# Performance work log

Measured on AMD Instinct MI355X. Metric: run time of the kernel, lower is better.

The kernel has to match this reference:

```python
import jax, jax.numpy as jnp
import numpy as np

BETA_2 = 1.0
LAMBDA_2 = 1.0


def _segment_logsumexp(x, seg, num_segments):
    # numerically stable segment logsumexp; empty segments -> 0.0
    m = jax.ops.segment_max(x, seg, num_segments=num_segments)
    m_safe = jnp.where(jnp.isfinite(m), m, 0.0)
    s = jax.ops.segment_sum(jnp.exp(x - m_safe[seg]), seg, num_segments=num_segments)
    lse = m_safe + jnp.log(s)
    return jnp.where(s > 0, lse, 0.0)


def setup_inputs() -> dict:
    key = jax.random.key(0)
    k1, k2, k3, k4, k5 = jax.random.split(key, 5)
    num_nodes, d, num_edges, num_graphs = 100000, 64, 3200000, 256
    Q2 = jax.random.normal(k1, (num_nodes, d), dtype=jnp.float32)
    K2 = jax.random.normal(k2, (num_nodes, d), dtype=jnp.float32)
    c_2 = jax.random.randint(k3, (num_edges,), 0, num_nodes)
    u_2 = jax.random.randint(k4, (num_edges,), 0, num_nodes)
    batch = jnp.sort(jax.random.randint(k5, (num_nodes,), 0, num_graphs))
    return {"Q2": Q2, "K2": K2, "c_2": c_2, "u_2": u_2, "batch": batch,
            "num_graphs": num_graphs}


def reference(Q2, K2, c_2, u_2, batch, num_graphs):
    num_nodes, d = Q2.shape
    scale = d ** 0.5
    # pairwise dot over edges: [E]
    ell_2 = jnp.sum(Q2[c_2] * K2[u_2], axis=-1) / scale
    # segment logsumexp grouped by destination node c: [N]
    lse_2 = _segment_logsumexp(BETA_2 * ell_2, c_2, num_nodes)
    # scatter-add per-node lse into per-graph energy: [G]
    graph_lse = jax.ops.segment_sum(lse_2, batch, num_segments=num_graphs)
    E = (LAMBDA_2 / BETA_2) * graph_lse
    return E
```

## Files before the change

kernel.cpp:

```cpp
#include <hip/hip_runtime.h>
#include <hip/hip_fp8.h>
#include <math.h>

typedef __attribute__((ext_vector_type(2))) float fv2;

#if defined(__has_builtin)
#  if __has_builtin(__builtin_amdgcn_cvt_pk_f32_fp8) && \
      __has_builtin(__builtin_amdgcn_cvt_pk_fp8_f32)
#    define PE_HAVE_FP8_BUILTINS 1
#  endif
#endif

#define MAX_NB 512
#define MAX_NB2 2048
#define UQ 4
#define NPB 256
#define NPB_SHIFT 8
#define B2_EPT 16
#define B2_CHUNK (B2_EPT * 256)
#define CPB 4
#define RT 1024
#define NXCD 8

__device__ __forceinline__ unsigned pack4_fp8(float a, float b, float c, float d) {
#ifdef PE_HAVE_FP8_BUILTINS
    int w = 0;
    w = __builtin_amdgcn_cvt_pk_fp8_f32(a, b, w, false);
    w = __builtin_amdgcn_cvt_pk_fp8_f32(c, d, w, true);
    return (unsigned)w;
#else
    unsigned r = 0;
    r |= (unsigned)__hip_fp8_e4m3(a).__x;
    r |= (unsigned)__hip_fp8_e4m3(b).__x << 8;
    r |= (unsigned)__hip_fp8_e4m3(c).__x << 16;
    r |= (unsigned)__hip_fp8_e4m3(d).__x << 24;
    return r;
#endif
}

__device__ __forceinline__ float dot4w_fp8(unsigned qa, unsigned ka, float acc) {
#ifdef PE_HAVE_FP8_BUILTINS
    fv2 q0 = __builtin_amdgcn_cvt_pk_f32_fp8((int)qa, false);
    fv2 q1 = __builtin_amdgcn_cvt_pk_f32_fp8((int)qa, true);
    fv2 k0 = __builtin_amdgcn_cvt_pk_f32_fp8((int)ka, false);
    fv2 k1 = __builtin_amdgcn_cvt_pk_f32_fp8((int)ka, true);
    acc = fmaf(q0.x, k0.x, acc);
    acc = fmaf(q0.y, k0.y, acc);
    acc = fmaf(q1.x, k1.x, acc);
    acc = fmaf(q1.y, k1.y, acc);
    return acc;
#else
#pragma unroll
    for (int j = 0; j < 4; ++j) {
        __hip_fp8_e4m3 qv, kv;
        qv.__x = (qa >> (8 * j)) & 0xff;
        kv.__x = (ka >> (8 * j)) & 0xff;
        acc = fmaf((float)qv, (float)kv, acc);
    }
    return acc;
#endif
}

__device__ __forceinline__ float dot16_fp8(const uint4& q, const uint4& k) {
    float d = 0.0f;
    d = dot4w_fp8(q.x, k.x, d);
    d = dot4w_fp8(q.y, k.y, d);
    d = dot4w_fp8(q.z, k.z, d);
    d = dot4w_fp8(q.w, k.w, d);
    return d;
}

__device__ __forceinline__ float red4(float d) {
    d += __shfl_xor(d, 1, 64);
    d += __shfl_xor(d, 2, 64);
    return d;
}

__device__ __forceinline__ int uquarter(int uu, int t1, int t2, int t3) {
    return (uu >= t1) + (uu >= t2) + (uu >= t3);
}

__global__ __launch_bounds__(256) void pe_convcount_kernel(
    const float* __restrict__ Q,
    const float* __restrict__ K,
    unsigned* __restrict__ Qq,
    unsigned* __restrict__ Kq,
    float* __restrict__ node_sum,
    float* __restrict__ out,
    const int* __restrict__ c,
    const int* __restrict__ u,
    unsigned* __restrict__ cnt_mat,
    int n4, int num_nodes, int num_graphs, int num_edges,
    int nb2, int nblk, int nconv,
    int t1, int t2, int t3) {
    __shared__ unsigned h[MAX_NB2];
    const int tid = threadIdx.x;

    if (blockIdx.x < nconv) {
        const int i = blockIdx.x * 256 + tid;
        if (i < num_nodes) node_sum[i] = 0.0f;
        if (i < num_graphs) out[i] = 0.0f;
        if (i >= n4) return;
        const float4 q = ((const float4*)Q)[i];
        const float4 k = ((const float4*)K)[i];
        Qq[i] = pack4_fp8(q.x, q.y, q.z, q.w);
        Kq[i] = pack4_fp8(k.x, k.y, k.z, k.w);
        return;
    }

    const int blk = blockIdx.x - nconv;
    for (int b = tid; b < nb2; b += 256) h[b] = 0u;
    __syncthreads();

    const int estart = blk * B2_CHUNK;
    const int ecount = min(B2_CHUNK, num_edges - estart);
    const int n4e = ecount >> 2;
    const int4* c4 = (const int4*)(c + estart);
    const int4* u4 = (const int4*)(u + estart);
    for (int k = tid; k < n4e; k += 256) {
        const int4 cv = c4[k];
        const int4 uv = u4[k];
        atomicAdd(&h[(cv.x >> NPB_SHIFT) * UQ + uquarter(uv.x, t1, t2, t3)], 1u);
        atomicAdd(&h[(cv.y >> NPB_SHIFT) * UQ + uquarter(uv.y, t1, t2, t3)], 1u);
        atomicAdd(&h[(cv.z >> NPB_SHIFT) * UQ + uquarter(uv.z, t1, t2, t3)], 1u);
        atomicAdd(&h[(cv.w >> NPB_SHIFT) * UQ + uquarter(uv.w, t1, t2, t3)], 1u);
    }
    for (int e = (n4e << 2) + tid; e < ecount; e += 256) {
        const int cc = c[estart + e];
        const int uu = u[estart + e];
        atomicAdd(&h[(cc >> NPB_SHIFT) * UQ + uquarter(uu, t1, t2, t3)], 1u);
    }
    __syncthreads();

    for (int b = tid; b < nb2; b += 256)
        cnt_mat[(size_t)b * nblk + blk] = h[b];
}

__global__ __launch_bounds__(256) void pe_matscan_kernel(
    unsigned* __restrict__ cnt_mat,
    unsigned* __restrict__ bin_cnt,
    int nblk) {
    __shared__ unsigned s[256];
    const int t = threadIdx.x;
    unsigned* row = cnt_mat + (size_t)blockIdx.x * nblk;
    unsigned carry = 0u;
    for (int t0 = 0; t0 < nblk; t0 += 256) {
        const int i = t0 + t;
        const unsigned v = (i < nblk) ? row[i] : 0u;
        s[t] = v;
        __syncthreads();
        for (int off = 1; off < 256; off <<= 1) {
            const unsigned mine = s[t];
            const unsigned add = (t >= off) ? s[t - off] : 0u;
            __syncthreads();
            s[t] = mine + add;
            __syncthreads();
        }
        if (i < nblk) row[i] = carry + (s[t] - v);
        carry += s[255];
        __syncthreads();
    }
    if (t == 0) bin_cnt[blockIdx.x] = carry;
}

__global__ __launch_bounds__(1024) void pe_scan_kernel(
    const unsigned* __restrict__ bin_cnt,
    unsigned* __restrict__ bin_base,
    int nb2) {
    __shared__ unsigned s[1024];
    const int t = threadIdx.x;
    const int i0 = 2 * t, i1 = 2 * t + 1;
    const unsigned v0 = (i0 < nb2) ? bin_cnt[i0] : 0u;
    const unsigned v1 = (i1 < nb2) ? bin_cnt[i1] : 0u;
    const unsigned p = v0 + v1;
    s[t] = p;
    __syncthreads();
    for (int off = 1; off < 1024; off <<= 1) {
        const unsigned mine = s[t];
        const unsigned add = (t >= off) ? s[t - off] : 0u;
        __syncthreads();
        s[t] = mine + add;
        __syncthreads();
    }
    const unsigned excl = s[t] - p;
    if (i0 < nb2) bin_base[i0] = excl;
    if (i1 < nb2) bin_base[i1] = excl + v0;
    if (t == 1023) bin_base[nb2] = s[1023];
}

__global__ __launch_bounds__(256) void pe_binify_kernel(
    const int* __restrict__ c,
    const int* __restrict__ u,
    const unsigned* __restrict__ cnt_mat,
    const unsigned* __restrict__ bin_base,
    unsigned* __restrict__ recs,
    int num_edges, int nb2, int nblk,
    int t1, int t2, int t3) {
    __shared__ unsigned rank[MAX_NB2];
    __shared__ unsigned lstart[MAX_NB2];
    __shared__ unsigned basesh[MAX_NB2];
    __shared__ unsigned srec[B2_CHUNK];
    __shared__ unsigned short sbuk[B2_CHUNK];
    __shared__ unsigned wtot[4];

    const int tid = threadIdx.x;
    const int blk = blockIdx.x;
    const int estart = blk * B2_CHUNK;
    const int ecount = min(B2_CHUNK, num_edges - estart);

    for (int b = tid; b < MAX_NB2; b += 256) rank[b] = 0u;
    for (int b = tid; b < nb2; b += 256)
        basesh[b] = bin_base[b] + cnt_mat[(size_t)b * nblk + blk];
    __syncthreads();

    unsigned rw[B2_EPT];
    int rb[B2_EPT];
    unsigned rr[B2_EPT];

    if (ecount == B2_CHUNK) {
        const int4* c4 = (const int4*)(c + estart);
        const int4* u4 = (const int4*)(u + estart);
#pragma unroll
        for (int jj = 0; jj < 4; ++jj) {
            const int k = jj * 256 + tid;
            const int4 cv = c4[k];
            const int4 uv = u4[k];
            const int j = jj * 4;
            rb[j + 0] = (cv.x >> NPB_SHIFT) * UQ + uquarter(uv.x, t1, t2, t3);
            rb[j + 1] = (cv.y >> NPB_SHIFT) * UQ + uquarter(uv.y, t1, t2, t3);
            rb[j + 2] = (cv.z >> NPB_SHIFT) * UQ + uquarter(uv.z, t1, t2, t3);
            rb[j + 3] = (cv.w >> NPB_SHIFT) * UQ + uquarter(uv.w, t1, t2, t3);
            rw[j + 0] = ((unsigned)uv.x << NPB_SHIFT) | (unsigned)(cv.x & (NPB - 1));
            rw[j + 1] = ((unsigned)uv.y << NPB_SHIFT) | (unsigned)(cv.y & (NPB - 1));
            rw[j + 2] = ((unsigned)uv.z << NPB_SHIFT) | (unsigned)(cv.z & (NPB - 1));
            rw[j + 3] = ((unsigned)uv.w << NPB_SHIFT) | (unsigned)(cv.w & (NPB - 1));
            rr[j + 0] = atomicAdd(&rank[rb[j + 0]], 1u);
            rr[j + 1] = atomicAdd(&rank[rb[j + 1]], 1u);
            rr[j + 2] = atomicAdd(&rank[rb[j + 2]], 1u);
            rr[j + 3] = atomicAdd(&rank[rb[j + 3]], 1u);
        }
    } else {
#pragma unroll
        for (int j = 0; j < B2_EPT; ++j) {
            rb[j] = -1;
            const int e = estart + j * 256 + tid;
            if (e < num_edges) {
                const int cc = c[e];
                const int uu = u[e];
                rb[j] = (cc >> NPB_SHIFT) * UQ + uquarter(uu, t1, t2, t3);
                rw[j] = ((unsigned)uu << NPB_SHIFT) | (unsigned)(cc & (NPB - 1));
                rr[j] = atomicAdd(&rank[rb[j]], 1u);
            }
        }
    }
    __syncthreads();

    {
        const int b8 = tid * 8;
        unsigned v[8];
        unsigned tsum = 0;
#pragma unroll
        for (int i = 0; i < 8; ++i) { v[i] = rank[b8 + i]; tsum += v[i]; }
        unsigned incl = tsum;
        const int lane = tid & 63;
#pragma unroll
        for (int off = 1; off < 64; off <<= 1) {
            const unsigned nv = __shfl_up(incl, off, 64);
            if (lane >= off) incl += nv;
        }
        if (lane == 63) wtot[tid >> 6] = incl;
        __syncthreads();
        unsigned woff = 0;
        const int w = tid >> 6;
        for (int i = 0; i < w; ++i) woff += wtot[i];
        unsigned run = woff + incl - tsum;
#pragma unroll
        for (int i = 0; i < 8; ++i) { lstart[b8 + i] = run; run += v[i]; }
    }
    __syncthreads();

#pragma unroll
    for (int j = 0; j < B2_EPT; ++j) {
        if (rb[j] >= 0) {
            const unsigned pos = lstart[rb[j]] + rr[j];
            srec[pos] = rw[j];
            sbuk[pos] = (unsigned short)rb[j];
        }
    }
    __syncthreads();

    for (int i = tid; i < ecount; i += 256) {
        const int b = sbuk[i];
        recs[basesh[b] + (unsigned)i - lstart[b]] = srec[i];
    }
}

__global__ __launch_bounds__(256) void pe_dotred_kernel(
    const unsigned* __restrict__ Qq,
    const unsigned* __restrict__ Kq,
    const unsigned* __restrict__ recs,
    const unsigned* __restrict__ bin_base,
    float* __restrict__ node_sum,
    int num_nodes, int nb) {
    __shared__ uint4 qlds[NPB * 4];
    __shared__ float acc[NPB];
    __shared__ unsigned rlds[RT];

    const int g = blockIdx.x;
    const int xcd = g & (NXCD - 1);
    const int slot = g >> 3;
    const int B = xcd + NXCD * (slot / CPB);
    const int chunk = slot - (slot / CPB) * CPB;
    if (B >= nb) return;

    const int t = threadIdx.x;
    const int gteam = t >> 2;
    const int sub = t & 3;
    const float inv_scale = 0.125f;

    const int nrows = min(NPB, num_nodes - B * NPB);
    const uint4* qsrc = (const uint4*)Qq + (size_t)B * NPB * 4;
    for (int i = t; i < nrows * 4; i += 256) qlds[i] = qsrc[i];
    acc[t] = 0.0f;

    const unsigned s0 = bin_base[B * UQ];
    const unsigned len = bin_base[B * UQ + UQ] - s0;
    const unsigned r0 = s0 + (unsigned)(((unsigned long long)len * chunk) / CPB);
    const unsigned r1 = s0 + (unsigned)(((unsigned long long)len * (chunk + 1)) / CPB);

    for (unsigned t0 = r0; t0 < r1; t0 += RT) {
        const unsigned n = min((unsigned)RT, r1 - t0);
        __syncthreads();
        for (unsigned i = t; i < n; i += 256) rlds[i] = recs[t0 + i];
        __syncthreads();
        for (unsigned i = gteam; i < n; i += 64) {
            const unsigned rec = rlds[i];
            const unsigned uu = rec >> NPB_SHIFT;
            const unsigned local = rec & (NPB - 1);
            const uint4 k = *(const uint4*)(Kq + (size_t)uu * 16 + sub * 4);
            const uint4 q = qlds[local * 4 + sub];
            const float d = red4(dot16_fp8(q, k));
            if (sub == 0) atomicAdd(&acc[local], __expf(d * inv_scale));
        }
    }
    __syncthreads();

    if (t < nrows && acc[t] != 0.0f)
        atomicAdd(&node_sum[B * NPB + t], acc[t]);
}

__global__ __launch_bounds__(256) void pe_node_kernel(
    const float* __restrict__ node_sum,
    const int* __restrict__ batch,
    float* __restrict__ out,
    int num_nodes) {
    const int n = blockIdx.x * blockDim.x + threadIdx.x;
    const bool valid = (n < num_nodes);
    const int nc = valid ? n : (num_nodes - 1);

    const float s = valid ? node_sum[nc] : 0.0f;
    float lse = (s > 0.0f) ? logf(s) : 0.0f;
    if (!valid) lse = 0.0f;
    const int b = batch[nc];

    const int b0 = __shfl(b, 0, 64);
    const bool uniform = __all(b == b0);
    if (uniform) {
        lse += __shfl_xor(lse, 1, 64);
        lse += __shfl_xor(lse, 2, 64);
        lse += __shfl_xor(lse, 4, 64);
        lse += __shfl_xor(lse, 8, 64);
        lse += __shfl_xor(lse, 16, 64);
        lse += __shfl_xor(lse, 32, 64);
        if ((threadIdx.x & 63) == 0 && lse != 0.0f) {
            atomicAdd(&out[b0], lse);
        }
    } else {
        if (valid && lse != 0.0f) {
            atomicAdd(&out[b], lse);
        }
    }
}


__global__ __launch_bounds__(256) void pe_convert_kernel(
    const float* __restrict__ Q,
    const float* __restrict__ K,
    unsigned* __restrict__ Qq,
    unsigned* __restrict__ Kq,
    float* __restrict__ node_sum,
    float* __restrict__ out,
    int n4, int num_nodes, int num_graphs) {
    const int i = blockIdx.x * blockDim.x + threadIdx.x;
    if (i < num_nodes) node_sum[i] = 0.0f;
    if (i < num_graphs) out[i] = 0.0f;
    if (i >= n4) return;
    const float4 q = ((const float4*)Q)[i];
    const float4 k = ((const float4*)K)[i];
    Qq[i] = pack4_fp8(q.x, q.y, q.z, q.w);
    Kq[i] = pack4_fp8(k.x, k.y, k.z, k.w);
}

__global__ __launch_bounds__(256) void pe_edge_kernel(
    const unsigned* __restrict__ Qq,
    const unsigned* __restrict__ Kq,
    const int* __restrict__ c,
    const int* __restrict__ u,
    float* __restrict__ node_sum,
    int num_edges) {
    const int tid = blockIdx.x * blockDim.x + threadIdx.x;
    const int group = tid >> 2;
    const int sub = tid & 3;
    const int ngroups = (gridDim.x * blockDim.x) >> 2;
    const float inv_scale = 0.125f;

    const int E4 = num_edges & ~3;

    for (int base = group * 4; base < E4; base += ngroups * 4) {
        const int4 ci = *(const int4*)(c + base);
        const int4 ui = *(const int4*)(u + base);

        const uint4 q0 = *(const uint4*)(Qq + (size_t)ci.x * 16 + sub * 4);
        const uint4 q1 = *(const uint4*)(Qq + (size_t)ci.y * 16 + sub * 4);
        const uint4 q2 = *(const uint4*)(Qq + (size_t)ci.z * 16 + sub * 4);
        const uint4 q3 = *(const uint4*)(Qq + (size_t)ci.w * 16 + sub * 4);
        const uint4 k0 = *(const uint4*)(Kq + (size_t)ui.x * 16 + sub * 4);
        const uint4 k1 = *(const uint4*)(Kq + (size_t)ui.y * 16 + sub * 4);
        const uint4 k2 = *(const uint4*)(Kq + (size_t)ui.z * 16 + sub * 4);
        const uint4 k3 = *(const uint4*)(Kq + (size_t)ui.w * 16 + sub * 4);

        float d0 = red4(dot16_fp8(q0, k0));
        float d1 = red4(dot16_fp8(q1, k1));
        float d2 = red4(dot16_fp8(q2, k2));
        float d3 = red4(dot16_fp8(q3, k3));

        const float dsel = (sub == 0) ? d0 : (sub == 1) ? d1 : (sub == 2) ? d2 : d3;
        const int csel = (sub == 0) ? ci.x : (sub == 1) ? ci.y : (sub == 2) ? ci.z : ci.w;
        atomicAdd(&node_sum[csel], __expf(dsel * inv_scale));
    }

    for (int e = E4 + group; e < num_edges; e += ngroups) {
        const int cc = c[e];
        const int uu = u[e];
        const uint4 q = *(const uint4*)(Qq + (size_t)cc * 16 + sub * 4);
        const uint4 k = *(const uint4*)(Kq + (size_t)uu * 16 + sub * 4);
        float d = red4(dot16_fp8(q, k));
        if (sub == 0) atomicAdd(&node_sum[cc], __expf(d * inv_scale));
    }
}

extern "C" void kernel_launch(void* const* d_in, const int* in_sizes, int n_in,
                              void* d_out, int out_size, void* d_ws, size_t ws_size,
                              hipStream_t stream) {
    const float* Q2 = (const float*)d_in[0];
    const float* K2 = (const float*)d_in[1];
    const int* c_2 = (const int*)d_in[2];
    const int* u_2 = (const int*)d_in[3];
    const int* batch = (const int*)d_in[4];

    const int num_nodes = in_sizes[4];
    const int num_edges = in_sizes[2];
    const int num_graphs = out_size;
    const int d = in_sizes[0] / num_nodes;
    const size_t row_elems = (size_t)num_nodes * d;
    const size_t row_bytes = row_elems;

    const int nb = (num_nodes + NPB - 1) >> NPB_SHIFT;
    const int nb2 = nb * UQ;
    const int nblk = (num_edges + B2_CHUNK - 1) / B2_CHUNK;

    const int t1 = num_nodes >> 2;
    const int t2 = num_nodes >> 1;
    const int t3 = t1 + t2;

    unsigned* Qq = (unsigned*)d_ws;
    unsigned* Kq = Qq + row_bytes / 4;
    unsigned* meta = Kq + row_bytes / 4;
    unsigned* bin_cnt = meta;
    unsigned* bin_base = meta + MAX_NB2;
    float* node_sum_b = (float*)(meta + 2 * MAX_NB2 + 16);
    const size_t ns_pad = ((size_t)num_nodes + 15) & ~(size_t)15;
    unsigned* recs = (unsigned*)node_sum_b + ns_pad;
    unsigned* cnt_mat = recs + num_edges;
    float* node_sum_f = (float*)meta;
    float* out = (float*)d_out;

    const size_t need_binned = row_bytes * 2 + (size_t)(2 * MAX_NB2 + 16) * 4 +
                               ns_pad * 4 + (size_t)num_edges * 4 +
                               (size_t)nb2 * nblk * 4;
    const bool use_binned = (nb <= MAX_NB) && (ws_size >= need_binned) &&
                            (d == 64) && (num_nodes <= (1 << 23));

    float* node_sum = use_binned ? node_sum_b : node_sum_f;
    const int n4 = (int)(row_elems / 4);
    const int nconv = (n4 + 255) / 256;

    if (use_binned) {
        pe_convcount_kernel<<<nconv + nblk, 256, 0, stream>>>(
            Q2, K2, Qq, Kq, node_sum, out, c_2, u_2, cnt_mat,
            n4, num_nodes, num_graphs, num_edges, nb2, nblk, nconv,
            t1, t2, t3);
        pe_matscan_kernel<<<nb2, 256, 0, stream>>>(cnt_mat, bin_cnt, nblk);
        pe_scan_kernel<<<1, 1024, 0, stream>>>(bin_cnt, bin_base, nb2);
        pe_binify_kernel<<<nblk, 256, 0, stream>>>(c_2, u_2, cnt_mat,
                                                   bin_base, recs,
                                                   num_edges, nb2, nblk,
                                                   t1, t2, t3);
        {
            const int grid = NXCD * ((nb + NXCD - 1) / NXCD) * CPB;
            pe_dotred_kernel<<<grid, 256, 0, stream>>>(Qq, Kq, recs,
                                                       bin_base,
                                                       node_sum, num_nodes, nb);
        }
    } else {
        pe_convert_kernel<<<nconv, 256, 0, stream>>>(
            Q2, K2, Qq, Kq, node_sum, out, n4, num_nodes, num_graphs);
        pe_edge_kernel<<<8192, 256, 0, stream>>>(Qq, Kq, c_2, u_2,
                                                 node_sum, num_edges);
    }

    {
        const int block = 256;
        const int grid = (num_nodes + block - 1) / block;
        pe_node_kernel<<<grid, block, 0, stream>>>(node_sum, batch, out,
                                                   num_nodes);
    }
}
```

Before: 236.8 us.

## Store per-block bin counts row-major and scan 16 columns per block

The per-chunk histogram matrix is transposed to block-major with padded rows, so the count kernel and binify write and read it contiguously. The column scan now processes 16 bins per workgroup using wave shuffles and vectorized uint4 loads instead of a 256-wide LDS scan per bin. The dot-reduce kernel drops its XCD-aware block swizzle and even splitting, and instead assigns one workgroup to each u-quarter sub-bin. That removes the strided cnt_mat accesses and many small scan launches, at the cost of possible load imbalance across quarters and lost L2 locality on each XCD.

Result: faster. 222.9 us (-5.9%).

```diff
diff --git a/kernel.cpp b/kernel.cpp
--- a/kernel.cpp
+++ b/kernel.cpp
@@ -18,9 +18,7 @@
 #define NPB_SHIFT 8
 #define B2_EPT 16
 #define B2_CHUNK (B2_EPT * 256)
-#define CPB 4
 #define RT 1024
-#define NXCD 8
 
 __device__ __forceinline__ unsigned pack4_fp8(float a, float b, float c, float d) {
 #ifdef PE_HAVE_FP8_BUILTINS
@@ -89,9 +87,9 @@
     float* __restrict__ out,
     const int* __restrict__ c,
     const int* __restrict__ u,
-    unsigned* __restrict__ cnt_mat,
+    unsigned* __restrict__ cnt,
     int n4, int num_nodes, int num_graphs, int num_edges,
-    int nb2, int nblk, int nconv,
+    int nb2p, int nblk, int nconv,
     int t1, int t2, int t3) {
     __shared__ unsigned h[MAX_NB2];
     const int tid = threadIdx.x;
@@ -109,7 +107,7 @@
     }
 
     const int blk = blockIdx.x - nconv;
-    for (int b = tid; b < nb2; b += 256) h[b] = 0u;
+    for (int b = tid; b < MAX_NB2; b += 256) h[b] = 0u;
     __syncthreads();
 
     const int estart = blk * B2_CHUNK;
@@ -132,35 +130,87 @@
     }
     __syncthreads();
 
-    for (int b = tid; b < nb2; b += 256)
-        cnt_mat[(size_t)b * nblk + blk] = h[b];
+    for (int b = tid; b < nb2p; b += 256)
+        cnt[(size_t)blk * nb2p + b] = h[b];
 }
 
 __global__ __launch_bounds__(256) void pe_matscan_kernel(
-    unsigned* __restrict__ cnt_mat,
+    unsigned* __restrict__ cnt,
     unsigned* __restrict__ bin_cnt,
-    int nblk) {
-    __shared__ unsigned s[256];
+    int nblk, int nb2p) {
+    __shared__ unsigned wsum[4][16];
     const int t = threadIdx.x;
-    unsigned* row = cnt_mat + (size_t)blockIdx.x * nblk;
-    unsigned carry = 0u;
+    const int lane = t & 63;
+    const int w = t >> 6;
+    const int col0 = blockIdx.x * 16;
+
+    unsigned carry[16];
+#pragma unroll
+    for (int i = 0; i < 16; ++i) carry[i] = 0u;
+
     for (int t0 = 0; t0 < nblk; t0 += 256) {
-        const int i = t0 + t;
-        const unsigned v = (i < nblk) ? row[i] : 0u;
-        s[t] = v;
-        __syncthreads();
-        for (int off = 1; off < 256; off <<= 1) {
-            const unsigned mine = s[t];
-            const unsigned add = (t >= off) ? s[t - off] : 0u;
-            __syncthreads();
-            s[t] = mine + add;
-            __syncthreads();
-        }
-        if (i < nblk) row[i] = carry + (s[t] - v);
-        carry += s[255];
-        __syncthreads();
-    }
-    if (t == 0) bin_cnt[blockIdx.x] = carry;
+        const int blk = t0 + t;
+        unsigned v[16], orig[16];
+        if (blk < nblk) {
+            const uint4* p = (const uint4*)(cnt + (size_t)blk * nb2p + col0);
+            const uint4 a = p[0], b = p[1], cc = p[2], dd = p[3];
+            v[0]=a.x;  v[1]=a.y;  v[2]=a.z;  v[3]=a.w;
+            v[4]=b.x;  v[5]=b.y;  v[6]=b.z;  v[7]=b.w;
+            v[8]=cc.x; v[9]=cc.y; v[10]=cc.z; v[11]=cc.w;
+            v[12]=dd.x; v[13]=dd.y; v[14]=dd.z; v[15]=dd.w;
+        } else {
+#pragma unroll
+            for (int i = 0; i < 16; ++i) v[i] = 0u;
+        }
+#pragma unroll
+        for (int i = 0; i < 16; ++i) orig[i] = v[i];
+
+#pragma unroll
+        for (int off = 1; off < 64; off <<= 1) {
+            unsigned nv[16];
+#pragma unroll
+            for (int i = 0; i < 16; ++i) nv[i] = __shfl_up(v[i], off, 64);
+            if (lane >= off) {
+#pragma unroll
+                for (int i = 0; i < 16; ++i) v[i] += nv[i];
+            }
+        }
+        if (lane == 63) {
+#pragma unroll
+            for (int i = 0; i < 16; ++i) wsum[w][i] = v[i];
+        }
+        __syncthreads();
+
+        unsigned woff[16];
+#pragma unroll
+        for (int i = 0; i < 16; ++i) woff[i] = 0u;
+        for (int ww = 0; ww < w; ++ww)
+#pragma unroll
+            for (int i = 0; i < 16; ++i) woff[i] += wsum[ww][i];
+
+        if (blk < nblk) {
+            uint4 o[4];
+            unsigned e[16];
+#pragma unroll
+            for (int i = 0; i < 16; ++i) e[i] = carry[i] + woff[i] + v[i] - orig[i];
+            o[0] = make_uint4(e[0], e[1], e[2], e[3]);
+            o[1] = make_uint4(e[4], e[5], e[6], e[7]);
+            o[2] = make_uint4(e[8], e[9], e[10], e[11]);
+            o[3] = make_uint4(e[12], e[13], e[14], e[15]);
+            uint4* p = (uint4*)(cnt + (size_t)blk * nb2p + col0);
+            p[0] = o[0]; p[1] = o[1]; p[2] = o[2]; p[3] = o[3];
+        }
+
+#pragma unroll
+        for (int i = 0; i < 16; ++i)
+            carry[i] += wsum[0][i] + wsum[1][i] + wsum[2][i] + wsum[3][i];
+        __syncthreads();
+    }
+
+    if (t == 0) {
+#pragma unroll
+        for (int i = 0; i < 16; ++i) bin_cnt[col0 + i] = carry[i];
+    }
 }
 
 __global__ __launch_bounds__(1024) void pe_scan_kernel(
@@ -191,10 +241,10 @@
 __global__ __launch_bounds__(256) void pe_binify_kernel(
     const int* __restrict__ c,
     const int* __restrict__ u,
-    const unsigned* __restrict__ cnt_mat,
+    const unsigned* __restrict__ cnt,
     const unsigned* __restrict__ bin_base,
     unsigned* __restrict__ recs,
-    int num_edges, int nb2, int nblk,
+    int num_edges, int nb2, int nb2p, int nblk,
     int t1, int t2, int t3) {
     __shared__ unsigned rank[MAX_NB2];
     __shared__ unsigned lstart[MAX_NB2];
@@ -210,7 +260,7 @@
 
     for (int b = tid; b < MAX_NB2; b += 256) rank[b] = 0u;
     for (int b = tid; b < nb2; b += 256)
-        basesh[b] = bin_base[b] + cnt_mat[(size_t)b * nblk + blk];
+        basesh[b] = bin_base[b] + cnt[(size_t)blk * nb2p + b];
     __syncthreads();
 
     unsigned rw[B2_EPT];
@@ -307,10 +357,8 @@
     __shared__ unsigned rlds[RT];
 
     const int g = blockIdx.x;
-    const int xcd = g & (NXCD - 1);
-    const int slot = g >> 3;
-    const int B = xcd + NXCD * (slot / CPB);
-    const int chunk = slot - (slot / CPB) * CPB;
+    const int B = g >> 2;
+    const int q = g & 3;
     if (B >= nb) return;
 
     const int t = threadIdx.x;
@@ -323,10 +371,8 @@
     for (int i = t; i < nrows * 4; i += 256) qlds[i] = qsrc[i];
     acc[t] = 0.0f;
 
-    const unsigned s0 = bin_base[B * UQ];
-    const unsigned len = bin_base[B * UQ + UQ] - s0;
-    const unsigned r0 = s0 + (unsigned)(((unsigned long long)len * chunk) / CPB);
-    const unsigned r1 = s0 + (unsigned)(((unsigned long long)len * (chunk + 1)) / CPB);
+    const unsigned r0 = bin_base[B * UQ + q];
+    const unsigned r1 = bin_base[B * UQ + q + 1];
 
     for (unsigned t0 = r0; t0 < r1; t0 += RT) {
         const unsigned n = min((unsigned)RT, r1 - t0);
@@ -338,8 +384,8 @@
             const unsigned uu = rec >> NPB_SHIFT;
             const unsigned local = rec & (NPB - 1);
             const uint4 k = *(const uint4*)(Kq + (size_t)uu * 16 + sub * 4);
-            const uint4 q = qlds[local * 4 + sub];
-            const float d = red4(dot16_fp8(q, k));
+            const uint4 q4 = qlds[local * 4 + sub];
+            const float d = red4(dot16_fp8(q4, k));
             if (sub == 0) atomicAdd(&acc[local], __expf(d * inv_scale));
         }
     }
@@ -467,6 +513,7 @@
 
     const int nb = (num_nodes + NPB - 1) >> NPB_SHIFT;
     const int nb2 = nb * UQ;
+    const int nb2p = (nb2 + 15) & ~15;
     const int nblk = (num_edges + B2_CHUNK - 1) / B2_CHUNK;
 
     const int t1 = num_nodes >> 2;
@@ -481,13 +528,13 @@
     float* node_sum_b = (float*)(meta + 2 * MAX_NB2 + 16);
     const size_t ns_pad = ((size_t)num_nodes + 15) & ~(size_t)15;
     unsigned* recs = (unsigned*)node_sum_b + ns_pad;
-    unsigned* cnt_mat = recs + num_edges;
+    unsigned* cnt = recs + num_edges;
     float* node_sum_f = (float*)meta;
     float* out = (float*)d_out;
 
     const size_t need_binned = row_bytes * 2 + (size_t)(2 * MAX_NB2 + 16) * 4 +
                                ns_pad * 4 + (size_t)num_edges * 4 +
-                               (size_t)nb2 * nblk * 4;
+                               (size_t)nblk * nb2p * 4;
     const bool use_binned = (nb <= MAX_NB) && (ws_size >= need_binned) &&
                             (d == 64) && (num_nodes <= (1 << 23));
 
@@ -497,21 +544,19 @@
 
     if (use_binned) {
         pe_convcount_kernel<<<nconv + nblk, 256, 0, stream>>>(
-            Q2, K2, Qq, Kq, node_sum, out, c_2, u_2, cnt_mat,
-            n4, num_nodes, num_graphs, num_edges, nb2, nblk, nconv,
+            Q2, K2, Qq, Kq, node_sum, out, c_2, u_2, cnt,
+            n4, num_nodes, num_graphs, num_edges, nb2p, nblk, nconv,
             t1, t2, t3);
-        pe_matscan_kernel<<<nb2, 256, 0, stream>>>(cnt_mat, bin_cnt, nblk);
+        pe_matscan_kernel<<<nb2p / 16, 256, 0, stream>>>(cnt, bin_cnt,
+                                                         nblk, nb2p);
         pe_scan_kernel<<<1, 1024, 0, stream>>>(bin_cnt, bin_base, nb2);
-        pe_binify_kernel<<<nblk, 256, 0, stream>>>(c_2, u_2, cnt_mat,
+        pe_binify_kernel<<<nblk, 256, 0, stream>>>(c_2, u_2, cnt,
                                                    bin_base, recs,
-                                                   num_edges, nb2, nblk,
+                                                   num_edges, nb2, nb2p, nblk,
                                                    t1, t2, t3);
-        {
-            const int grid = NXCD * ((nb + NXCD - 1) / NXCD) * CPB;
-            pe_dotred_kernel<<<grid, 256, 0, stream>>>(Qq, Kq, recs,
-                                                       bin_base,
-                                                       node_sum, num_nodes, nb);
-        }
+        pe_dotred_kernel<<<nb * UQ, 256, 0, stream>>>(Qq, Kq, recs,
+                                                      bin_base,
+                                                      node_sum, num_nodes, nb);
     } else {
         pe_convert_kernel<<<nconv, 256, 0, stream>>>(
             Q2, K2, Qq, Kq, node_sum, out, n4, num_nodes, num_graphs);
```
